# Kernel optimization log

Hardware: AMD Instinct MI355X
Metric: run time of the kernel (lower is better)

The kernel has to match this reference:

```python
import jax, jax.numpy as jnp
import numpy as np

NUM_NEURONS = 256
NUM_SAMPLES = 512
MAX_SPIKES = 32
N_STEPS = 32          # fixed RK4 steps per spike round (stands in for adaptive Tsit5)
ALPHA = 0.03
V_RESET = 1.0
T0 = 0.0


def setup_inputs() -> dict:
    key = jax.random.key(0)
    ks = jax.random.split(key, 7)
    input_current = jax.random.normal(ks[0], (NUM_NEURONS,), dtype=jnp.float32)
    # _build_w with network=all-False: uniform(minval=0.5), mask sets nothing
    w = jax.random.uniform(ks[1], (NUM_NEURONS, NUM_NEURONS), minval=0.5, maxval=1.0, dtype=jnp.float32)
    mu = jax.random.uniform(ks[2], (2,), minval=0.5, maxval=1.0, dtype=jnp.float32)
    v0 = jax.random.normal(ks[3], (NUM_NEURONS,), dtype=jnp.float32)
    i0 = jax.random.normal(ks[4], (NUM_NEURONS,), dtype=jnp.float32)
    # s0 = log(U) - alpha  (always < 0)
    s0 = (jnp.log(jax.random.uniform(ks[5], (NUM_SAMPLES, NUM_NEURONS), minval=1e-6, maxval=1.0)) - ALPHA).astype(jnp.float32)
    # pre-drawn stochastic resets, one per (spike round, sample, neuron)
    reset_s = (jnp.log(jax.random.uniform(ks[6], (MAX_SPIKES, NUM_SAMPLES, NUM_NEURONS), minval=1e-6, maxval=1.0)) - ALPHA).astype(jnp.float32)
    return dict(input_current=input_current, w=w, mu=mu, v0=v0, i0=i0, s0=s0, reset_s=reset_s, t1=2)


def _drift(y, ic, mu1, mu2):
    # y: [samples, neurons, 3] = (v, i, s)
    v, i = y[..., 0], y[..., 1]
    dv = mu1 * (i + ic - v)
    di = -mu2 * i
    ds = jax.nn.sigmoid(v)  # intensity_fn(v)
    return jnp.stack([dv, di, ds], axis=-1)


def reference(input_current, w, mu, v0, i0, s0, reset_s, t1):
    t1f = jnp.float32(t1)
    mu1, mu2 = mu[0], mu[1]
    ic = input_current  # constant-in-time input current, [neurons]

    y0 = jnp.concatenate([
        jnp.broadcast_to(v0, (NUM_SAMPLES, NUM_NEURONS))[..., None],
        jnp.broadcast_to(i0, (NUM_SAMPLES, NUM_NEURONS))[..., None],
        s0[..., None]], axis=-1)  # [samples, neurons, 3]

    def rk4(y, h):
        k1 = _drift(y, ic, mu1, mu2)
        k2 = _drift(y + 0.5 * h * k1, ic, mu1, mu2)
        k3 = _drift(y + 0.5 * h * k2, ic, mu1, mu2)
        k4 = _drift(y + h * k3, ic, mu1, mu2)
        return y + (h / 6.0) * (k1 + 2.0 * k2 + 2.0 * k3 + k4)

    def round_body(carry, reset_k):
        t0s, y_in = carry                      # t0s: [samples]
        dt = (t1f - t0s) / N_STEPS             # per-sample step size
        h = dt[:, None, None]

        def step(sc, _):
            t, y, done, tev, yev, emask = sc
            y_new = rk4(y, h)
            y_new = jnp.where(done[:, None, None], y, y_new)  # freeze after event
            s_prev, s_new = y[..., 2], y_new[..., 2]
            crossed = s_new > 0.0                              # cond_fn root: s crosses 0
            trig = crossed.any(axis=1) & (~done)
            idx = jnp.argmax(s_new, axis=1)                    # event neuron (first/largest crossing)
            sp = jnp.take_along_axis(s_prev, idx[:, None], 1)[:, 0]
            sn = jnp.take_along_axis(s_new, idx[:, None], 1)[:, 0]
            frac = jnp.clip(sp / (sp - sn + 1e-12), 0.0, 1.0)  # linear root estimate (Newton stand-in)
            t_c = t + frac * dt
            y_c = y + frac[:, None, None] * (y_new - y)
            tev = jnp.where(trig, t_c, tev)
            yev = jnp.where(trig[:, None, None], y_c, yev)
            emask = jnp.where(trig[:, None], crossed, emask)
            y = jnp.where(trig[:, None, None], y_c, y_new)
            done = done | trig
            return (t + dt, y, done, tev, yev, emask), None

        done0 = jnp.zeros((NUM_SAMPLES,), bool)
        tev0 = jnp.full((NUM_SAMPLES,), jnp.inf, jnp.float32)
        em0 = jnp.zeros((NUM_SAMPLES, NUM_NEURONS), bool)
        (_, yend, done, tev, yev, emask), _ = jax.lax.scan(
            step, (t0s, y_in, done0, tev0, y_in, em0), None, length=N_STEPS)

        tev = jnp.where(done, tev, t1f)                 # no event -> sol.ts[-1] = t1
        yev = jnp.where(done[:, None, None], yev, yend)

        # trans_fn: spike reset + synaptic jump w[event_idx]
        eidx = jnp.argmax(emask, axis=1)
        w_row = jnp.where(done[:, None], w[eidx], 0.0)  # zero if no event happened
        v_t = yev[..., 0] - jnp.where(emask, V_RESET, 0.0)
        i_t = yev[..., 1] + w_row
        s_t = jnp.minimum(jnp.where(emask, reset_k, yev[..., 2]), 0.0)
        y_next = jnp.stack([v_t, i_t, s_t], axis=-1)
        return (tev, y_next), (tev, yev, emask)

    t0s = jnp.full((NUM_SAMPLES,), T0, jnp.float32)
    _, (tevs, yevs, emasks) = jax.lax.scan(jax.checkpoint(round_body), (t0s, y0), reset_s)

    spike_times = jnp.transpose(tevs, (1, 0))            # [samples, max_spikes]
    spike_values = jnp.transpose(yevs, (1, 0, 2, 3))     # [samples, max_spikes, neurons, 3]
    spike_marks = jnp.transpose(emasks, (1, 0, 2))       # [samples, max_spikes, neurons]
    return spike_times, spike_values, spike_marks
```

## Files before the change

### kernel.cpp

```cpp
#include <hip/hip_runtime.h>
#include <math.h>

#define NN 256
#define NS 512
#define MS 32
#define NSTEP 32
#define VRESET 1.0f

__device__ __forceinline__ float sigf(float x) {
    float e = __expf(-x);
    return __builtin_amdgcn_rcpf(1.0f + e);
}

__device__ __forceinline__ void block_sync_lds() {
    asm volatile("s_waitcnt lgkmcnt(0)" ::: "memory");
    __builtin_amdgcn_s_barrier();
    asm volatile("" ::: "memory");
}

__device__ __forceinline__ void rk4step(float v, float ii, float s,
                                        float ic, float mu1, float mu2,
                                        float dt, float hh, float h6,
                                        float& vn, float& in_, float& sn)
{
    float kv1 = mu1 * (ii + ic - v);
    float ki1 = -mu2 * ii;
    float ks1 = sigf(v);
    float v2 = v + hh * kv1;
    float i2 = ii + hh * ki1;
    float kv2 = mu1 * (i2 + ic - v2);
    float ki2 = -mu2 * i2;
    float ks2 = sigf(v2);
    float v3 = v + hh * kv2;
    float i3 = ii + hh * ki2;
    float kv3 = mu1 * (i3 + ic - v3);
    float ki3 = -mu2 * i3;
    float ks3 = sigf(v3);
    float v4 = v + dt * kv3;
    float i4 = ii + dt * ki3;
    float kv4 = mu1 * (i4 + ic - v4);
    float ki4 = -mu2 * i4;
    float ks4 = sigf(v4);
    vn  = v  + h6 * (kv1 + 2.0f * kv2 + 2.0f * kv3 + kv4);
    in_ = ii + h6 * (ki1 + 2.0f * ki2 + 2.0f * ki3 + ki4);
    sn  = s  + h6 * (ks1 + 2.0f * ks2 + 2.0f * ks3 + ks4);
}

__global__ __launch_bounds__(256) void snn_kernel(
    const float* __restrict__ ic_g,
    const float* __restrict__ w,
    const float* __restrict__ mu,
    const float* __restrict__ v0,
    const float* __restrict__ i0,
    const float* __restrict__ s0,
    const float* __restrict__ reset_s,
    const int*   __restrict__ t1p,
    float* __restrict__ out)
{
    const int tid  = threadIdx.x;
    const int lane = tid & 63;
    const int wid  = tid >> 6;
    const int samp = blockIdx.x;
    const float mu1 = mu[0];
    const float mu2 = mu[1];
    const float t1f = (float)t1p[0];

    __shared__ int4 s_flag[4][4];

    float v  = v0[tid];
    float ii = i0[tid];
    float s  = s0[samp * NN + tid];
    const float ic = ic_g[tid];
    float t0 = 0.0f;

    float* times = out;
    float* vals  = out + (size_t)NS * MS;
    float* marks = out + (size_t)NS * MS * (1 + NN * 3);

    for (int r = 0; r < MS; ++r) {
        const float rs = reset_s[((size_t)r * NS + samp) * NN + tid];

        const float dt = (t1f - t0) / (float)NSTEP;
        float tev = t1f;
        float yv = v, yi = ii, ys = s;
        bool  em = false;
        bool  done = false;
        float wr = 0.0f;

        if (dt != 0.0f) {
            const float hh = 0.5f * dt;
            const float h6 = dt * (1.0f / 6.0f);

            float pv = v, pi_ = ii, ps = s;
            float cv, ci, cs;
            rk4step(pv, pi_, ps, ic, mu1, mu2, dt, hh, h6, cv, ci, cs);
            float t = t0;

            for (int st = 0; st < NSTEP; ++st) {
                unsigned long long bl = __ballot(cs > 0.0f);
                unsigned csb  = __float_as_uint(cs);
                unsigned okey = (csb & 0x80000000u) ? ~csb
                                                    : (csb | 0x80000000u);
                unsigned red = okey;
#pragma unroll
                for (int off = 32; off >= 1; off >>= 1) {
                    unsigned o = __shfl_xor(red, off);
                    red = (o > red) ? o : red;
                }
                unsigned long long wm = __ballot(okey == red);
                int   winlane = (int)__builtin_ctzll(wm);
                float wps = __shfl(ps, winlane);
                float wcs = __shfl(cs, winlane);
                if (lane == 0) {
                    int mincross = (bl != 0ull)
                        ? ((wid << 6) + (int)__builtin_ctzll(bl)) : 0x1FF;
                    int4 e;
                    e.x = (int)red;
                    e.y = (mincross << 1) | ((bl != 0ull) ? 1 : 0);
                    e.z = __float_as_int(wps);
                    e.w = __float_as_int(wcs);
                    s_flag[st & 3][wid] = e;
                }

                float kv1 = mu1 * (ci + ic - cv);
                float ki1 = -mu2 * ci;
                float ks1 = sigf(cv);
                float v2 = cv + hh * kv1;
                float i2 = ci + hh * ki1;
                float kv2 = mu1 * (i2 + ic - v2);
                float ki2 = -mu2 * i2;
                float ks2 = sigf(v2);

                __builtin_amdgcn_sched_barrier(0);
                block_sync_lds();
                __builtin_amdgcn_sched_barrier(0);

                int4 f0 = s_flag[st & 3][0];
                int4 f1 = s_flag[st & 3][1];
                int4 f2 = s_flag[st & 3][2];
                int4 f3 = s_flag[st & 3][3];

                float v3 = cv + hh * kv2;
                float i3 = ci + hh * ki2;
                float kv3 = mu1 * (i3 + ic - v3);
                float ki3 = -mu2 * i3;
                float ks3 = sigf(v3);
                float v4 = cv + dt * kv3;
                float i4 = ci + dt * ki3;
                float kv4 = mu1 * (i4 + ic - v4);
                float ki4 = -mu2 * i4;
                float ks4 = sigf(v4);
                float nv  = cv + h6 * (kv1 + 2.0f * kv2 + 2.0f * kv3 + kv4);
                float ni  = ci + h6 * (ki1 + 2.0f * ki2 + 2.0f * ki3 + ki4);
                float ns_ = cs + h6 * (ks1 + 2.0f * ks2 + 2.0f * ks3 + ks4);

                if ((f0.y | f1.y | f2.y | f3.y) & 1) {
                    int e0 = (f0.y & 1) ? ((f0.y >> 1) & 0x1FF) : 512;
                    int e1 = (f1.y & 1) ? ((f1.y >> 1) & 0x1FF) : 512;
                    int e2 = (f2.y & 1) ? ((f2.y >> 1) & 0x1FF) : 512;
                    int e3 = (f3.y & 1) ? ((f3.y >> 1) & 0x1FF) : 512;
                    int ea = e0 < e1 ? e0 : e1;
                    int eb = e2 < e3 ? e2 : e3;
                    int eidx = ea < eb ? ea : eb;
                    wr = w[eidx * NN + tid];

                    unsigned bk = (unsigned)f0.x;
                    float bsp = __int_as_float(f0.z);
                    float bv  = __int_as_float(f0.w);
                    if ((unsigned)f1.x > bk) { bk = (unsigned)f1.x;
                        bsp = __int_as_float(f1.z); bv = __int_as_float(f1.w); }
                    if ((unsigned)f2.x > bk) { bk = (unsigned)f2.x;
                        bsp = __int_as_float(f2.z); bv = __int_as_float(f2.w); }
                    if ((unsigned)f3.x > bk) { bk = (unsigned)f3.x;
                        bsp = __int_as_float(f3.z); bv = __int_as_float(f3.w); }

                    float frac = bsp / (bsp - bv + 1e-12f);
                    frac = fminf(fmaxf(frac, 0.0f), 1.0f);
                    tev = t + frac * dt;
                    yv = pv  + frac * (cv - pv);
                    yi = pi_ + frac * (ci - pi_);
                    ys = ps  + frac * (cs - ps);
                    em = (cs > 0.0f);
                    done = true;
                    break;
                }

                if (st + 1 < NSTEP) {
                    pv = cv; pi_ = ci; ps = cs;
                    cv = nv; ci = ni; cs = ns_;
                    t += dt;
                }
            }

            if (!done) { yv = cv; yi = ci; ys = cs; }
        }

        const int sr = samp * MS + r;
        if (tid == 0) times[sr] = tev;
        {
            float* p = vals + ((size_t)sr * NN + tid) * 3;
            p[0] = yv;
            p[1] = yi;
            p[2] = ys;
            marks[(size_t)sr * NN + tid] = em ? 1.0f : 0.0f;
        }

        if (done) {
            v  = yv - (em ? VRESET : 0.0f);
            ii = yi + wr;
            float sres = em ? rs : ys;
            s = fminf(sres, 0.0f);
        } else {
            v = yv; ii = yi;
            s = fminf(ys, 0.0f);
        }
        t0 = tev;
    }
}

extern "C" void kernel_launch(void* const* d_in, const int* in_sizes, int n_in,
                              void* d_out, int out_size, void* d_ws, size_t ws_size,
                              hipStream_t stream) {
    const float* ic      = (const float*)d_in[0];
    const float* w       = (const float*)d_in[1];
    const float* mu      = (const float*)d_in[2];
    const float* v0      = (const float*)d_in[3];
    const float* i0      = (const float*)d_in[4];
    const float* s0      = (const float*)d_in[5];
    const float* reset_s = (const float*)d_in[6];
    const int*   t1p     = (const int*)d_in[7];
    float* out = (float*)d_out;

    snn_kernel<<<dim3(NS), dim3(256), 0, stream>>>(ic, w, mu, v0, i0, s0,
                                                   reset_s, t1p, out);
}
```

Measured before the change: 138.0 us.

## Restructure RK4 event loop to overlap full next step before barrier check

Reorganizes the per-step loop so the full next RK4 step is computed before the previously published event summary is checked. The barrier and publish of the new step's summary then come after that compute, which pipelines the block-wide reduction latency behind a whole RK4 step instead of half of one. Event handling is hoisted out of the loop and uses the A/B state triple. This adds an extra barrier for the first step and one step of wasted compute per round when an event is found.

```diff
diff --git a/kernel.cpp b/kernel.cpp
--- a/kernel.cpp
+++ b/kernel.cpp
@@ -46,6 +46,35 @@
     sn  = s  + h6 * (ks1 + 2.0f * ks2 + 2.0f * ks3 + ks4);
 }
 
+__device__ __forceinline__ void publish_summary(float curS, float prevS,
+                                                int lane, int wid,
+                                                int4* slotp)
+{
+    unsigned long long bl = __ballot(curS > 0.0f);
+    unsigned b = __float_as_uint(curS);
+    unsigned okey = (b & 0x80000000u) ? ~b : (b | 0x80000000u);
+    unsigned red = okey;
+#pragma unroll
+    for (int off = 32; off >= 1; off >>= 1) {
+        unsigned o = __shfl_xor(red, off);
+        red = (o > red) ? o : red;
+    }
+    unsigned long long wm = __ballot(okey == red);
+    int   winlane = (int)__builtin_ctzll(wm);
+    float wps = __shfl(prevS, winlane);
+    float wcs = __shfl(curS, winlane);
+    if (lane == 0) {
+        int mincross = (bl != 0ull)
+            ? ((wid << 6) + (int)__builtin_ctzll(bl)) : 0x1FF;
+        int4 e;
+        e.x = (int)red;
+        e.y = (mincross << 1) | ((bl != 0ull) ? 1 : 0);
+        e.z = __float_as_int(wps);
+        e.w = __float_as_int(wcs);
+        slotp[wid] = e;
+    }
+}
+
 __global__ __launch_bounds__(256) void snn_kernel(
     const float* __restrict__ ic_g,
     const float* __restrict__ w,
@@ -65,7 +94,7 @@
     const float mu2 = mu[1];
     const float t1f = (float)t1p[0];
 
-    __shared__ int4 s_flag[4][4];
+    __shared__ int4 s_flag[6][4];
 
     float v  = v0[tid];
     float ii = i0[tid];
@@ -91,108 +120,76 @@
             const float hh = 0.5f * dt;
             const float h6 = dt * (1.0f / 6.0f);
 
-            float pv = v, pi_ = ii, ps = s;
-            float cv, ci, cs;
-            rk4step(pv, pi_, ps, ic, mu1, mu2, dt, hh, h6, cv, ci, cs);
+            float Av = v, Ai = ii, As = s;
+            float Bv, Bi, Bs;
+            rk4step(Av, Ai, As, ic, mu1, mu2, dt, hh, h6, Bv, Bi, Bs);
+
+            publish_summary(Bs, As, lane, wid, s_flag[4 + (r & 1)]);
+            block_sync_lds();
+            int4 p0 = s_flag[4 + (r & 1)][0];
+            int4 p1 = s_flag[4 + (r & 1)][1];
+            int4 p2 = s_flag[4 + (r & 1)][2];
+            int4 p3 = s_flag[4 + (r & 1)][3];
+            __builtin_amdgcn_sched_barrier(0);
+
             float t = t0;
-
-            for (int st = 0; st < NSTEP; ++st) {
-                unsigned long long bl = __ballot(cs > 0.0f);
-                unsigned csb  = __float_as_uint(cs);
-                unsigned okey = (csb & 0x80000000u) ? ~csb
-                                                    : (csb | 0x80000000u);
-                unsigned red = okey;
-#pragma unroll
-                for (int off = 32; off >= 1; off >>= 1) {
-                    unsigned o = __shfl_xor(red, off);
-                    red = (o > red) ? o : red;
-                }
-                unsigned long long wm = __ballot(okey == red);
-                int   winlane = (int)__builtin_ctzll(wm);
-                float wps = __shfl(ps, winlane);
-                float wcs = __shfl(cs, winlane);
-                if (lane == 0) {
-                    int mincross = (bl != 0ull)
-                        ? ((wid << 6) + (int)__builtin_ctzll(bl)) : 0x1FF;
-                    int4 e;
-                    e.x = (int)red;
-                    e.y = (mincross << 1) | ((bl != 0ull) ? 1 : 0);
-                    e.z = __float_as_int(wps);
-                    e.w = __float_as_int(wcs);
-                    s_flag[st & 3][wid] = e;
-                }
-
-                float kv1 = mu1 * (ci + ic - cv);
-                float ki1 = -mu2 * ci;
-                float ks1 = sigf(cv);
-                float v2 = cv + hh * kv1;
-                float i2 = ci + hh * ki1;
-                float kv2 = mu1 * (i2 + ic - v2);
-                float ki2 = -mu2 * i2;
-                float ks2 = sigf(v2);
-
+            float Cv, Ci, Cs;
+
+            for (int st = 1; st < NSTEP; ++st) {
+                rk4step(Bv, Bi, Bs, ic, mu1, mu2, dt, hh, h6, Cv, Ci, Cs);
                 __builtin_amdgcn_sched_barrier(0);
-                block_sync_lds();
-                __builtin_amdgcn_sched_barrier(0);
-
-                int4 f0 = s_flag[st & 3][0];
-                int4 f1 = s_flag[st & 3][1];
-                int4 f2 = s_flag[st & 3][2];
-                int4 f3 = s_flag[st & 3][3];
-
-                float v3 = cv + hh * kv2;
-                float i3 = ci + hh * ki2;
-                float kv3 = mu1 * (i3 + ic - v3);
-                float ki3 = -mu2 * i3;
-                float ks3 = sigf(v3);
-                float v4 = cv + dt * kv3;
-                float i4 = ci + dt * ki3;
-                float kv4 = mu1 * (i4 + ic - v4);
-                float ki4 = -mu2 * i4;
-                float ks4 = sigf(v4);
-                float nv  = cv + h6 * (kv1 + 2.0f * kv2 + 2.0f * kv3 + kv4);
-                float ni  = ci + h6 * (ki1 + 2.0f * ki2 + 2.0f * ki3 + ki4);
-                float ns_ = cs + h6 * (ks1 + 2.0f * ks2 + 2.0f * ks3 + ks4);
-
-                if ((f0.y | f1.y | f2.y | f3.y) & 1) {
-                    int e0 = (f0.y & 1) ? ((f0.y >> 1) & 0x1FF) : 512;
-                    int e1 = (f1.y & 1) ? ((f1.y >> 1) & 0x1FF) : 512;
-                    int e2 = (f2.y & 1) ? ((f2.y >> 1) & 0x1FF) : 512;
-                    int e3 = (f3.y & 1) ? ((f3.y >> 1) & 0x1FF) : 512;
-                    int ea = e0 < e1 ? e0 : e1;
-                    int eb = e2 < e3 ? e2 : e3;
-                    int eidx = ea < eb ? ea : eb;
-                    wr = w[eidx * NN + tid];
-
-                    unsigned bk = (unsigned)f0.x;
-                    float bsp = __int_as_float(f0.z);
-                    float bv  = __int_as_float(f0.w);
-                    if ((unsigned)f1.x > bk) { bk = (unsigned)f1.x;
-                        bsp = __int_as_float(f1.z); bv = __int_as_float(f1.w); }
-                    if ((unsigned)f2.x > bk) { bk = (unsigned)f2.x;
-                        bsp = __int_as_float(f2.z); bv = __int_as_float(f2.w); }
-                    if ((unsigned)f3.x > bk) { bk = (unsigned)f3.x;
-                        bsp = __int_as_float(f3.z); bv = __int_as_float(f3.w); }
-
-                    float frac = bsp / (bsp - bv + 1e-12f);
-                    frac = fminf(fmaxf(frac, 0.0f), 1.0f);
-                    tev = t + frac * dt;
-                    yv = pv  + frac * (cv - pv);
-                    yi = pi_ + frac * (ci - pi_);
-                    ys = ps  + frac * (cs - ps);
-                    em = (cs > 0.0f);
+
+                if ((p0.y | p1.y | p2.y | p3.y) & 1) {
                     done = true;
                     break;
                 }
 
-                if (st + 1 < NSTEP) {
-                    pv = cv; pi_ = ci; ps = cs;
-                    cv = nv; ci = ni; cs = ns_;
-                    t += dt;
-                }
+                publish_summary(Cs, Bs, lane, wid, s_flag[(st + 1) & 3]);
+                block_sync_lds();
+                p0 = s_flag[(st + 1) & 3][0];
+                p1 = s_flag[(st + 1) & 3][1];
+                p2 = s_flag[(st + 1) & 3][2];
+                p3 = s_flag[(st + 1) & 3][3];
+                __builtin_amdgcn_sched_barrier(0);
+
+                Av = Bv; Ai = Bi; As = Bs;
+                Bv = Cv; Bi = Ci; Bs = Cs;
+                t += dt;
             }
 
-            if (!done) { yv = cv; yi = ci; ys = cs; }
+            if (!done) {
+                if ((p0.y | p1.y | p2.y | p3.y) & 1) done = true;
+                else { yv = Bv; yi = Bi; ys = Bs; }
+            }
+
+            if (done) {
+                int e0 = (p0.y & 1) ? ((p0.y >> 1) & 0x1FF) : 512;
+                int e1 = (p1.y & 1) ? ((p1.y >> 1) & 0x1FF) : 512;
+                int e2 = (p2.y & 1) ? ((p2.y >> 1) & 0x1FF) : 512;
+                int e3 = (p3.y & 1) ? ((p3.y >> 1) & 0x1FF) : 512;
+                int ea = e0 < e1 ? e0 : e1;
+                int eb = e2 < e3 ? e2 : e3;
+                int eidx = ea < eb ? ea : eb;
+                wr = w[eidx * NN + tid];
+
+                unsigned bk = (unsigned)p0.x;
+                float bsp = __int_as_float(p0.z);
+                float bv  = __int_as_float(p0.w);
+                if ((unsigned)p1.x > bk) { bk = (unsigned)p1.x;
+                    bsp = __int_as_float(p1.z); bv = __int_as_float(p1.w); }
+                if ((unsigned)p2.x > bk) { bk = (unsigned)p2.x;
+                    bsp = __int_as_float(p2.z); bv = __int_as_float(p2.w); }
+                if ((unsigned)p3.x > bk) { bk = (unsigned)p3.x;
+                    bsp = __int_as_float(p3.z); bv = __int_as_float(p3.w); }
+
+                float frac = bsp / (bsp - bv + 1e-12f);
+                frac = fminf(fmaxf(frac, 0.0f), 1.0f);
+                tev = t + frac * dt;
+                yv = Av + frac * (Bv - Av);
+                yi = Ai + frac * (Bi - Ai);
+                ys = As + frac * (Bs - As);
+                em = (Bs > 0.0f);
+            }
         }
 
         const int sr = samp * MS + r;
```

Result: faster. 134.0 us (-2.9%).
